# Kernel optimization log

Hardware: AMD Instinct MI355X
Metric: run time of the kernel (lower is better)

The kernel has to match this reference:

```python
import jax, jax.numpy as jnp
import numpy as np

B, T, V, D, P, DEP = 64, 32, 32000, 1024, 8, 4
TAU = 1.0
EPS = 1e-5


def setup_inputs() -> dict:
    key = jax.random.key(0)
    ks = jax.random.split(key, 9)
    s = 0.02
    x = jax.random.randint(ks[0], (B, T), 0, V)
    emb = jax.random.normal(ks[1], (V, D), jnp.float32) * s
    pos = jax.random.normal(ks[2], (T, D), jnp.float32) * s
    # primitive library: n_prims MLPs (Linear -> GELU -> Linear), stacked
    w1 = jax.random.normal(ks[3], (P, D, D), jnp.float32) * s
    b1 = jnp.zeros((P, D), jnp.float32)
    w2 = jax.random.normal(ks[4], (P, D, D), jnp.float32) * s
    b2 = jnp.zeros((P, D), jnp.float32)
    # one selector Linear(dim, n_prims) per depth
    sel_w = jax.random.normal(ks[5], (DEP, P, D), jnp.float32) * s
    sel_b = jnp.zeros((DEP, P), jnp.float32)
    ln_g = jnp.ones((D,), jnp.float32)
    ln_b = jnp.zeros((D,), jnp.float32)
    head_w = jax.random.normal(ks[6], (V, D), jnp.float32) * s
    # fixed gumbel noise (replaces torch's in-op sampling, kept deterministic)
    u = jax.random.uniform(ks[7], (DEP, B, P), jnp.float32, 1e-6, 1.0 - 1e-6)
    gumbel = -jnp.log(-jnp.log(u))
    return dict(x=x, emb=emb, pos=pos, w1=w1, b1=b1, w2=w2, b2=b2,
                sel_w=sel_w, sel_b=sel_b, ln_g=ln_g, ln_b=ln_b,
                head_w=head_w, gumbel=gumbel)


def reference(x, emb, pos, w1, b1, w2, b2, sel_w, sel_b, ln_g, ln_b, head_w, gumbel):
    h = emb[x] + pos[None, :x.shape[1], :]          # [B,T,D]
    div = jnp.float32(0.0)
    unif = jnp.float32(1.0 / P)
    for d in range(DEP):
        ctx = h.mean(axis=1)                         # [B,D]
        logits = ctx @ sel_w[d].T + sel_b[d]         # [B,P]
        weights = jax.nn.softmax((logits + gumbel[d]) / TAU, axis=-1)
        # all primitives over all tokens at once (grouped GEMM), no T loop
        u1 = jax.nn.gelu(jnp.einsum('btd,pde->btpe', h, w1) + b1, approximate=False)
        prim = jnp.einsum('btpe,pef->btpf', u1, w2) + b2   # [B,T,P,D]
        h = h + jnp.einsum('btpf,bp->btf', prim, weights)  # residual add
        avg = weights.mean(axis=0)                   # [P]
        # F.kl_div(avg.log(), uniform, reduction='sum')
        div = div + jnp.sum(unif * (jnp.log(unif) - jnp.log(avg)))
    mu = h.mean(-1, keepdims=True)
    var = ((h - mu) ** 2).mean(-1, keepdims=True)
    hn = (h - mu) * jax.lax.rsqrt(var + EPS) * ln_g + ln_b
    return hn @ head_w.T, div
```

## Files before the change

### kernel.cpp

```cpp
#include <hip/hip_runtime.h>
#include <hip/hip_bf16.h>
#include <math.h>

typedef __bf16 bf16x8 __attribute__((ext_vector_type(8)));
typedef float  f32x4  __attribute__((ext_vector_type(4)));

struct __align__(8) bf16x4s { __hip_bfloat16 a, b, c, d; };

__device__ __forceinline__ void gload_lds16(const void* g, void* l) {
  __builtin_amdgcn_global_load_lds(
      (const __attribute__((address_space(1))) void*)g,
      (__attribute__((address_space(3))) void*)l, 16, 0, 0);
}

__device__ __forceinline__ float fast_gelu(float v) {
  float s = 0.70710678118654752f * v;
  float a = fabsf(s);
  float t = __builtin_amdgcn_rcpf(fmaf(0.3275911f, a, 1.0f));
  float p = t * fmaf(t, fmaf(t, fmaf(t, fmaf(t, 1.061405429f, -1.453152027f),
                                     1.421413741f), -0.284496736f), 0.254829592f);
  float e = __expf(-a * a);
  float er = copysignf(fmaf(-p, e, 1.0f), s);
  return 0.5f * v * (1.0f + er);
}

#define BAR()   asm volatile("s_barrier" ::: "memory")
#define LGKM0() do { asm volatile("s_waitcnt lgkmcnt(0)" ::: "memory"); \
                     __builtin_amdgcn_sched_barrier(0); } while (0)
#define LGKM8() do { asm volatile("s_waitcnt lgkmcnt(8)" ::: "memory"); \
                     __builtin_amdgcn_sched_barrier(0); } while (0)
#define VMC(N)  do { asm volatile("s_waitcnt vmcnt(" #N ")" ::: "memory"); \
                     __builtin_amdgcn_sched_barrier(0); } while (0)
#define P1()    __builtin_amdgcn_s_setprio(1)
#define P0()    __builtin_amdgcn_s_setprio(0)

#define MQ(MB, NB, AV, BV)                                                    \
  do {                                                                        \
    _Pragma("unroll")                                                         \
    for (int mi_ = 0; mi_ < 4; ++mi_)                                         \
      _Pragma("unroll")                                                       \
      for (int nj_ = 0; nj_ < 2; ++nj_)                                       \
        _Pragma("unroll")                                                     \
        for (int kk_ = 0; kk_ < 2; ++kk_)                                     \
          acc[MB + mi_][NB + nj_] = __builtin_amdgcn_mfma_f32_16x16x32_bf16(  \
              AV[mi_][kk_], BV[nj_][kk_], acc[MB + mi_][NB + nj_], 0, 0, 0);  \
  } while (0)

template<int EPI>
__global__ __launch_bounds__(512, 2)
void gemm_nt(const __hip_bfloat16* __restrict__ A,
             const __hip_bfloat16* __restrict__ B,
             const int K, const int Kc, const int N,
             const float* __restrict__ p0,
             const float* __restrict__ p1,
             float* __restrict__ f32out,
             __hip_bfloat16* __restrict__ bfout)
{
  __shared__ __align__(16) __hip_bfloat16 lds[65536];

  const int tid = threadIdx.x;
  const int lane = tid & 63, wid = tid >> 6;
  const int l15 = lane & 15, l4 = lane >> 4;
  const int r8 = lane >> 3, blk = lane & 7;
  const int wm = wid >> 2, wn = wid & 3;

  const int nx = gridDim.x;
  const int flat = blockIdx.x + nx * blockIdx.y;
  const int q = (nx * gridDim.y) >> 3;
  const int nid = (flat & 7) * q + (flat >> 3);
  const long m0 = (long)(nid % nx) * 256;
  const long n0 = (long)(nid / nx) * 256;

  const int kbeg = blockIdx.z * Kc;
  const int nt = Kc / 64;

  f32x4 acc[8][4] = {};
  bf16x8 arE[4][2], arL[4][2], brE[2][2], brL[2][2];

  auto stageA = [&](int buf, int h, int k0) {
#pragma unroll
    for (int p2 = 0; p2 < 2; ++p2) {
      int ch = p2 * 16 + h * 8 + wid;
      int row = ch * 8 + r8;
      gload_lds16(A + (m0 + row) * (long)K + k0 + ((blk ^ r8) << 3),
                  lds + buf * 16384 + ch * 512);
    }
  };
  auto stageB = [&](int buf, int h, int k0) {
#pragma unroll
    for (int p2 = 0; p2 < 2; ++p2) {
      int ch = (p2 * 2 + (wid >> 2)) * 8 + h * 4 + (wid & 3);
      int row = ch * 8 + r8;
      gload_lds16(B + (n0 + row) * (long)K + k0 + ((blk ^ r8) << 3),
                  lds + 32768 + buf * 16384 + ch * 512);
    }
  };
  auto readAE = [&](int buf) {
    const __hip_bfloat16* pA = lds + buf * 16384;
#pragma unroll
    for (int mi = 0; mi < 4; ++mi)
#pragma unroll
      for (int kk = 0; kk < 2; ++kk) {
        int row = wm * 128 + mi * 16 + l15;
        arE[mi][kk] = *(const bf16x8*)(pA + row * 64 + (((kk * 4 + l4) ^ (row & 7)) << 3));
      }
  };
  auto readAL = [&](int buf) {
    const __hip_bfloat16* pA = lds + buf * 16384;
#pragma unroll
    for (int mi = 0; mi < 4; ++mi)
#pragma unroll
      for (int kk = 0; kk < 2; ++kk) {
        int row = wm * 128 + 64 + mi * 16 + l15;
        arL[mi][kk] = *(const bf16x8*)(pA + row * 64 + (((kk * 4 + l4) ^ (row & 7)) << 3));
      }
  };
  auto readBE = [&](int buf) {
    const __hip_bfloat16* pB = lds + 32768 + buf * 16384;
#pragma unroll
    for (int nj = 0; nj < 2; ++nj)
#pragma unroll
      for (int kk = 0; kk < 2; ++kk) {
        int row = wn * 64 + nj * 16 + l15;
        brE[nj][kk] = *(const bf16x8*)(pB + row * 64 + (((kk * 4 + l4) ^ (row & 7)) << 3));
      }
  };
  auto readBL = [&](int buf) {
    const __hip_bfloat16* pB = lds + 32768 + buf * 16384;
#pragma unroll
    for (int nj = 0; nj < 2; ++nj)
#pragma unroll
      for (int kk = 0; kk < 2; ++kk) {
        int row = wn * 64 + 32 + nj * 16 + l15;
        brL[nj][kk] = *(const bf16x8*)(pB + row * 64 + (((kk * 4 + l4) ^ (row & 7)) << 3));
      }
  };

  stageA(0, 0, kbeg); stageB(0, 0, kbeg); stageB(0, 1, kbeg); stageA(0, 1, kbeg);
  VMC(4);
  stageA(1, 0, kbeg + 64); stageB(1, 0, kbeg + 64); stageB(1, 1, kbeg + 64);
  VMC(6);
  BAR();

  const int nit = nt >> 1;
  for (int t = 0; t < nit; ++t) {
    const bool fl = (t + 1 < nit);
    const int kA = kbeg + (2 * t + 1) * 64;
    const int kB = kbeg + (2 * t + 2) * 64;
    const int kC = kbeg + (2 * t + 3) * 64;
    readAE(0); readBE(0);
    stageA(1, 1, kA);
    LGKM8();
    BAR(); LGKM0();
    P1(); MQ(0, 0, arE, brE); P0();
    BAR();
    readBL(0);
    if (fl) stageA(0, 0, kB);
    BAR(); LGKM0();
    P1(); MQ(0, 2, arE, brL); P0();
    BAR();
    readAL(0);
    if (fl) stageB(0, 0, kB);
    BAR(); LGKM0();
    P1(); MQ(4, 0, arL, brE); P0();
    BAR();
    if (fl) stageB(0, 1, kB);
    BAR();
    P1(); MQ(4, 2, arL, brL); P0();
    if (fl) { VMC(6); } else { VMC(0); }
    BAR();
    readAE(1); readBE(1);
    if (fl) stageA(0, 1, kB);
    LGKM8();
    BAR(); LGKM0();
    P1(); MQ(0, 0, arE, brE); P0();
    BAR();
    readBL(1);
    if (fl) stageA(1, 0, kC);
    BAR(); LGKM0();
    P1(); MQ(0, 2, arE, brL); P0();
    BAR();
    readAL(1);
    if (fl) stageB(1, 0, kC);
    BAR(); LGKM0();
    P1(); MQ(4, 0, arL, brE); P0();
    BAR();
    if (fl) stageB(1, 1, kC);
    BAR();
    P1(); MQ(4, 2, arL, brL); P0();
    if (fl) VMC(6);
    BAR();
  }

  const long slab = (EPI == 4) ? (long)blockIdx.z * (long)(gridDim.x * 256) * N : 0;
#pragma unroll
  for (int mi = 0; mi < 8; ++mi) {
    const long gmb = m0 + wm * 128 + mi * 16 + l4 * 4;
    const int b = (int)(gmb >> 5);
#pragma unroll
    for (int nj = 0; nj < 4; ++nj) {
      const long gn = n0 + wn * 64 + nj * 16 + l15;
      if constexpr (EPI == 0) {
        const int p = (int)(gn >> 10), e = (int)(gn & 1023);
        const float bias = p0[(p << 10) + e];
        const float wpb = p1[(b << 3) + p];
#pragma unroll
        for (int r = 0; r < 4; ++r) {
          float v = fast_gelu(acc[mi][nj][r] + bias) * wpb;
          bfout[(gmb + r) * (long)N + gn] = __float2bfloat16(v);
        }
      } else if constexpr (EPI == 2) {
#pragma unroll
        for (int r = 0; r < 4; ++r)
          f32out[(gmb + r) * (long)N + gn] = acc[mi][nj][r];
      } else {
#pragma unroll
        for (int r = 0; r < 4; ++r)
          bfout[slab + (gmb + r) * (long)N + gn] = __float2bfloat16(acc[mi][nj][r]);
      }
    }
  }
}

__global__ void cvt_bf16_k(const float* __restrict__ in, __hip_bfloat16* __restrict__ out, long n) {
  long i = ((long)blockIdx.x * blockDim.x + threadIdx.x) * 4;
  if (i >= n) return;
  float4 v = *(const float4*)(in + i);
  *(bf16x4s*)(out + i) = bf16x4s{__float2bfloat16(v.x), __float2bfloat16(v.y),
                                 __float2bfloat16(v.z), __float2bfloat16(v.w)};
}

__global__ void tconv_k(const float* __restrict__ in, __hip_bfloat16* __restrict__ out,
                        long in_bs, long out_rs, long out_bs) {
  __shared__ float tile[32][33];
  int p = blockIdx.z;
  int r0 = blockIdx.y * 32, c0 = blockIdx.x * 32;
  int tx = threadIdx.x, ty = threadIdx.y;
#pragma unroll
  for (int i = 0; i < 32; i += 8)
    tile[ty + i][tx] = in[(long)p * in_bs + (long)(r0 + ty + i) * 1024 + c0 + tx];
  __syncthreads();
#pragma unroll
  for (int i = 0; i < 32; i += 8)
    out[(long)(c0 + ty + i) * out_rs + (long)p * out_bs + (r0 + tx)] =
        __float2bfloat16(tile[tx][ty + i]);
}

__global__ void embed_k(const int* __restrict__ x, const float* __restrict__ emb,
                        const float* __restrict__ pos, float* __restrict__ h,
                        __hip_bfloat16* __restrict__ hb, float* __restrict__ divp) {
  int row = blockIdx.x;
  int t = row & 31;
  int c = threadIdx.x * 4;
  long tok = x[row];
  float4 e = *(const float4*)(emb + tok * 1024 + c);
  float4 q = *(const float4*)(pos + (long)t * 1024 + c);
  float4 v{e.x + q.x, e.y + q.y, e.z + q.z, e.w + q.w};
  *(float4*)(h + (long)row * 1024 + c) = v;
  *(bf16x4s*)(hb + (long)row * 1024 + c) =
      bf16x4s{__float2bfloat16(v.x), __float2bfloat16(v.y),
              __float2bfloat16(v.z), __float2bfloat16(v.w)};
  if (row == 0 && threadIdx.x == 0) *divp = 0.f;
}

__global__ void select_wb2_k(const float* __restrict__ h, const float* __restrict__ selw,
                             const float* __restrict__ selb, const float* __restrict__ gum,
                             const float* __restrict__ b2, float* __restrict__ W,
                             float* __restrict__ wb2, int dep) {
  int b = blockIdx.x, tid = threadIdx.x;
  int c = tid * 4;
  float4 s{0.f, 0.f, 0.f, 0.f};
  for (int t = 0; t < 32; ++t) {
    const float4 v = *(const float4*)(h + ((long)(b * 32 + t)) * 1024 + c);
    s.x += v.x; s.y += v.y; s.z += v.z; s.w += v.w;
  }
  float lp[8];
#pragma unroll
  for (int p = 0; p < 8; ++p) {
    const float4 w = *(const float4*)(selw + dep * 8192 + p * 1024 + c);
    lp[p] = (s.x * w.x + s.y * w.y + s.z * w.z + s.w * w.w) * (1.f / 32.f);
  }
  int lane = tid & 63, wid = tid >> 6;
#pragma unroll
  for (int p = 0; p < 8; ++p)
    for (int o = 32; o; o >>= 1) lp[p] += __shfl_down(lp[p], o);
  __shared__ float red[4][8];
  __shared__ float wsm[8];
  if (lane == 0) {
#pragma unroll
    for (int p = 0; p < 8; ++p) red[wid][p] = lp[p];
  }
  __syncthreads();
  if (tid == 0) {
    float lg[8], mx = -1e30f;
    for (int p = 0; p < 8; ++p) {
      lg[p] = red[0][p] + red[1][p] + red[2][p] + red[3][p]
            + selb[dep * 8 + p] + gum[dep * 512 + b * 8 + p];
      mx = fmaxf(mx, lg[p]);
    }
    float sm = 0.f;
    for (int p = 0; p < 8; ++p) { lg[p] = expf(lg[p] - mx); sm += lg[p]; }
    float inv = 1.f / sm;
    for (int p = 0; p < 8; ++p) { wsm[p] = lg[p] * inv; W[dep * 512 + b * 8 + p] = lg[p] * inv; }
  }
  __syncthreads();
  float4 a{0.f, 0.f, 0.f, 0.f};
#pragma unroll
  for (int p = 0; p < 8; ++p) {
    float wp = wsm[p];
    const float4 v = *(const float4*)(b2 + p * 1024 + c);
    a.x += wp * v.x; a.y += wp * v.y; a.z += wp * v.z; a.w += wp * v.w;
  }
  *(float4*)(wb2 + (long)b * 1024 + c) = a;
}

__global__ void h_update_k(const __hip_bfloat16* __restrict__ part, float* __restrict__ h,
                           const float* __restrict__ wb2, __hip_bfloat16* __restrict__ hb,
                           const float* __restrict__ Wd, float* __restrict__ divp) {
  int row = blockIdx.x * 2 + (threadIdx.x >> 7);
  int c = (threadIdx.x & 127) * 8;
  long idx = (long)row * 1024 + c;
  float4 a0 = *(const float4*)(h + idx);
  float4 a1 = *(const float4*)(h + idx + 4);
  const float4 w0 = *(const float4*)(wb2 + (long)(row >> 5) * 1024 + c);
  const float4 w1 = *(const float4*)(wb2 + (long)(row >> 5) * 1024 + c + 4);
  a0.x += w0.x; a0.y += w0.y; a0.z += w0.z; a0.w += w0.w;
  a1.x += w1.x; a1.y += w1.y; a1.z += w1.z; a1.w += w1.w;
#pragma unroll
  for (int s = 0; s < 8; ++s) {
    const bf16x8 v = *(const bf16x8*)(part + (long)s * 2097152 + idx);
    a0.x += (float)v[0]; a0.y += (float)v[1]; a0.z += (float)v[2]; a0.w += (float)v[3];
    a1.x += (float)v[4]; a1.y += (float)v[5]; a1.z += (float)v[6]; a1.w += (float)v[7];
  }
  *(float4*)(h + idx) = a0;
  *(float4*)(h + idx + 4) = a1;
  bf16x8 ob;
  ob[0] = (__bf16)a0.x; ob[1] = (__bf16)a0.y; ob[2] = (__bf16)a0.z; ob[3] = (__bf16)a0.w;
  ob[4] = (__bf16)a1.x; ob[5] = (__bf16)a1.y; ob[6] = (__bf16)a1.z; ob[7] = (__bf16)a1.w;
  *(bf16x8*)(hb + idx) = ob;
  if (blockIdx.x == 0 && threadIdx.x < 64) {
    float w8[8];
#pragma unroll
    for (int p = 0; p < 8; ++p) w8[p] = Wd[threadIdx.x * 8 + p];
#pragma unroll
    for (int p = 0; p < 8; ++p)
      for (int o = 32; o; o >>= 1) w8[p] += __shfl_down(w8[p], o);
    if (threadIdx.x == 0) {
      float d = *divp;
      const float u = 0.125f, lu = logf(0.125f);
#pragma unroll
      for (int p = 0; p < 8; ++p) d += u * (lu - logf(w8[p] * (1.f / 64.f)));
      *divp = d;
    }
  }
}

__global__ void ln_k(const float* __restrict__ h, const float* __restrict__ g,
                     const float* __restrict__ be, __hip_bfloat16* __restrict__ hnb,
                     const float* __restrict__ divp, float* __restrict__ divout) {
  int row = blockIdx.x, tid = threadIdx.x;
  int c = tid * 4;
  const float4 v = *(const float4*)(h + (long)row * 1024 + c);
  float s = v.x + v.y + v.z + v.w;
  float q = v.x * v.x + v.y * v.y + v.z * v.z + v.w * v.w;
  for (int o = 32; o; o >>= 1) { s += __shfl_down(s, o); q += __shfl_down(q, o); }
  __shared__ float red[16];
  int lane = tid & 63, wid = tid >> 6;
  if (lane == 0) { red[wid] = s; red[8 + wid] = q; }
  __syncthreads();
  if (tid == 0) {
    float S = red[0] + red[1] + red[2] + red[3];
    float Q = red[8] + red[9] + red[10] + red[11];
    float mu = S * (1.f / 1024.f);
    float var = Q * (1.f / 1024.f) - mu * mu;
    red[0] = mu; red[1] = rsqrtf(var + 1e-5f);
  }
  __syncthreads();
  float mu = red[0], rs = red[1];
  float4 gg = *(const float4*)(g + c), bb = *(const float4*)(be + c);
  *(bf16x4s*)(hnb + (long)row * 1024 + c) =
      bf16x4s{__float2bfloat16((v.x - mu) * rs * gg.x + bb.x),
              __float2bfloat16((v.y - mu) * rs * gg.y + bb.y),
              __float2bfloat16((v.z - mu) * rs * gg.z + bb.z),
              __float2bfloat16((v.w - mu) * rs * gg.w + bb.w)};
  if (row == 0 && tid == 0) *divout = *divp;
}

extern "C" void kernel_launch(void* const* d_in, const int* in_sizes, int n_in,
                              void* d_out, int out_size, void* d_ws, size_t ws_size,
                              hipStream_t stream) {
  (void)in_sizes; (void)n_in; (void)out_size; (void)ws_size;
  const int*   x     = (const int*)  d_in[0];
  const float* emb   = (const float*)d_in[1];
  const float* pos   = (const float*)d_in[2];
  const float* w1    = (const float*)d_in[3];
  const float* b1    = (const float*)d_in[4];
  const float* w2    = (const float*)d_in[5];
  const float* b2    = (const float*)d_in[6];
  const float* selw  = (const float*)d_in[7];
  const float* selb  = (const float*)d_in[8];
  const float* lng   = (const float*)d_in[9];
  const float* lnb   = (const float*)d_in[10];
  const float* headw = (const float*)d_in[11];
  const float* gum   = (const float*)d_in[12];
  float* out = (float*)d_out;

  char* ws = (char*)d_ws;
  __hip_bfloat16* w1t   = (__hip_bfloat16*)(ws);
  __hip_bfloat16* w2t   = (__hip_bfloat16*)(ws + 16777216);
  __hip_bfloat16* headb = (__hip_bfloat16*)(ws + 33554432);
  float*          h     = (float*)(ws + 99090432);
  __hip_bfloat16* hb    = (__hip_bfloat16*)(ws + 107479040);
  __hip_bfloat16* u1    = (__hip_bfloat16*)(ws + 111673344);
  float*          Wall  = (float*)(ws + 145227776);
  float*          wb2   = (float*)(ws + 145240064);
  float*          divp  = (float*)(ws + 145502208);
  __hip_bfloat16* part  = (__hip_bfloat16*)out;

  cvt_bf16_k<<<32000, 256, 0, stream>>>(headw, headb, 32768000L);
  tconv_k<<<dim3(32, 32, 8), dim3(32, 8), 0, stream>>>(w1, w1t, 1L << 20, 1024L, 1L << 20);
  tconv_k<<<dim3(32, 32, 8), dim3(32, 8), 0, stream>>>(w2, w2t, 1L << 20, 8192L, 1024L);
  embed_k<<<2048, 256, 0, stream>>>(x, emb, pos, h, hb, divp);

  for (int d = 0; d < 4; ++d) {
    select_wb2_k<<<64, 256, 0, stream>>>(h, selw, selb, gum, b2, Wall, wb2, d);
    gemm_nt<0><<<dim3(8, 32), 512, 0, stream>>>(hb, w1t, 1024, 1024, 8192, b1, Wall + d * 512, nullptr, u1);
    gemm_nt<4><<<dim3(8, 4, 8), 512, 0, stream>>>(u1, w2t, 8192, 1024, 1024, nullptr, nullptr, nullptr, part);
    h_update_k<<<1024, 256, 0, stream>>>(part, h, wb2, hb, Wall + d * 512, divp);
  }

  ln_k<<<2048, 256, 0, stream>>>(h, lng, lnb, hb, divp, out + 65536000L);
  gemm_nt<2><<<dim3(8, 125), 512, 0, stream>>>(hb, headb, 1024, 1024, 32000, nullptr, nullptr, out, nullptr);
}
```

Baseline: 606.9 us.

## Add dedicated head GEMM loading B operand directly to registers

Replaces the generic gemm_nt instantiation for the final vocabulary projection with a specialized gemm_head kernel. Only the A (activation) tile is staged through LDS, double-buffered with swizzling. The B (head weight) fragments are loaded straight from global memory into registers, also double-buffered, and a flat-to-tile swizzle groups blocks for L2 reuse. This halves the LDS footprint and removes LDS round-trips for B, at the cost of higher register pressure (launch bounds drop to 1 block per CU) and uncoalesced global B reads.

```diff
diff --git a/kernel.cpp b/kernel.cpp
--- a/kernel.cpp
+++ b/kernel.cpp
@@ -46,6 +46,18 @@
               AV[mi_][kk_], BV[nj_][kk_], acc[MB + mi_][NB + nj_], 0, 0, 0);  \
   } while (0)
 
+#define MQH(MB, NB, AV, BV)                                                   \
+  do {                                                                        \
+    _Pragma("unroll")                                                         \
+    for (int mi_ = 0; mi_ < 4; ++mi_)                                         \
+      _Pragma("unroll")                                                       \
+      for (int nj_ = 0; nj_ < 2; ++nj_)                                       \
+        _Pragma("unroll")                                                     \
+        for (int kk_ = 0; kk_ < 2; ++kk_)                                     \
+          acc[MB + mi_][NB + nj_] = __builtin_amdgcn_mfma_f32_16x16x32_bf16(  \
+              AV[mi_][kk_], BV[NB + nj_][kk_], acc[MB + mi_][NB + nj_], 0, 0, 0); \
+  } while (0)
+
 template<int EPI>
 __global__ __launch_bounds__(512, 2)
 void gemm_nt(const __hip_bfloat16* __restrict__ A,
@@ -209,15 +221,130 @@
           float v = fast_gelu(acc[mi][nj][r] + bias) * wpb;
           bfout[(gmb + r) * (long)N + gn] = __float2bfloat16(v);
         }
-      } else if constexpr (EPI == 2) {
-#pragma unroll
-        for (int r = 0; r < 4; ++r)
-          f32out[(gmb + r) * (long)N + gn] = acc[mi][nj][r];
       } else {
 #pragma unroll
         for (int r = 0; r < 4; ++r)
           bfout[slab + (gmb + r) * (long)N + gn] = __float2bfloat16(acc[mi][nj][r]);
       }
+    }
+  }
+}
+
+__global__ __launch_bounds__(512, 1)
+void gemm_head(const __hip_bfloat16* __restrict__ A,
+               const __hip_bfloat16* __restrict__ B,
+               const int K, const int N, float* __restrict__ f32out)
+{
+  __shared__ __align__(16) __hip_bfloat16 lds[32768];
+
+  const int tid = threadIdx.x;
+  const int lane = tid & 63, wid = tid >> 6;
+  const int l15 = lane & 15, l4 = lane >> 4;
+  const int r8 = lane >> 3, blk = lane & 7;
+  const int wm = wid >> 2, wn = wid & 3;
+
+  const int nx = gridDim.x;
+  const int flat = blockIdx.x + nx * blockIdx.y;
+  const int q = (nx * gridDim.y) >> 3;
+  const int nid = (flat & 7) * q + (flat >> 3);
+  const long m0 = (long)(nid % nx) * 256;
+  const long n0 = (long)(nid / nx) * 256;
+
+  const int nt = K / 64;
+
+  f32x4 acc[8][4] = {};
+  bf16x8 ar[4][2];
+  bf16x8 b0[4][2], b1[4][2];
+
+  auto stageA2 = [&](int buf, int k0) {
+#pragma unroll
+    for (int p2 = 0; p2 < 4; ++p2) {
+      int ch = p2 * 8 + wid;
+      int row = ch * 8 + r8;
+      gload_lds16(A + (m0 + row) * (long)K + k0 + ((blk ^ r8) << 3),
+                  lds + buf * 16384 + ch * 512);
+    }
+  };
+  auto loadB = [&](bf16x8 (&bb)[4][2], int k0) {
+#pragma unroll
+    for (int nj = 0; nj < 4; ++nj)
+#pragma unroll
+      for (int kk = 0; kk < 2; ++kk)
+        bb[nj][kk] = *(const bf16x8*)(B + (n0 + wn * 64 + nj * 16 + l15) * (long)K
+                                        + k0 + kk * 32 + l4 * 8);
+  };
+  auto readAE = [&](int buf) {
+    const __hip_bfloat16* pA = lds + buf * 16384;
+#pragma unroll
+    for (int mi = 0; mi < 4; ++mi)
+#pragma unroll
+      for (int kk = 0; kk < 2; ++kk) {
+        int row = wm * 128 + mi * 16 + l15;
+        ar[mi][kk] = *(const bf16x8*)(pA + row * 64 + (((kk * 4 + l4) ^ (row & 7)) << 3));
+      }
+  };
+  auto readAL = [&](int buf) {
+    const __hip_bfloat16* pA = lds + buf * 16384;
+#pragma unroll
+    for (int mi = 0; mi < 4; ++mi)
+#pragma unroll
+      for (int kk = 0; kk < 2; ++kk) {
+        int row = wm * 128 + 64 + mi * 16 + l15;
+        ar[mi][kk] = *(const bf16x8*)(pA + row * 64 + (((kk * 4 + l4) ^ (row & 7)) << 3));
+      }
+  };
+
+  stageA2(0, 0);
+  loadB(b0, 0);
+  stageA2(1, 64);
+  VMC(12);
+  BAR();
+  readAE(0);
+
+  const int nit = nt >> 1;
+  for (int t = 0; t < nit - 1; ++t) {
+    loadB(b1, (2 * t + 1) * 64);
+    P1(); MQH(0, 0, ar, b0); MQH(0, 2, ar, b0); P0();
+    readAL(0);
+    P1(); MQH(4, 0, ar, b0); MQH(4, 2, ar, b0); P0();
+    LGKM0();
+    BAR();
+    stageA2(0, (2 * t + 2) * 64);
+    VMC(12);
+    BAR();
+    readAE(1);
+    loadB(b0, (2 * t + 2) * 64);
+    P1(); MQH(0, 0, ar, b1); MQH(0, 2, ar, b1); P0();
+    readAL(1);
+    P1(); MQH(4, 0, ar, b1); MQH(4, 2, ar, b1); P0();
+    LGKM0();
+    BAR();
+    stageA2(1, (2 * t + 3) * 64);
+    VMC(12);
+    BAR();
+    readAE(0);
+  }
+
+  loadB(b1, (nt - 1) * 64);
+  P1(); MQH(0, 0, ar, b0); MQH(0, 2, ar, b0); P0();
+  readAL(0);
+  P1(); MQH(4, 0, ar, b0); MQH(4, 2, ar, b0); P0();
+  VMC(8);
+  BAR();
+  readAE(1);
+  P1(); MQH(0, 0, ar, b1); MQH(0, 2, ar, b1); P0();
+  readAL(1);
+  P1(); MQH(4, 0, ar, b1); MQH(4, 2, ar, b1); P0();
+
+#pragma unroll
+  for (int mi = 0; mi < 8; ++mi) {
+    const long gmb = m0 + wm * 128 + mi * 16 + l4 * 4;
+#pragma unroll
+    for (int nj = 0; nj < 4; ++nj) {
+      const long gn = n0 + wn * 64 + nj * 16 + l15;
+#pragma unroll
+      for (int r = 0; r < 4; ++r)
+        f32out[(gmb + r) * (long)N + gn] = acc[mi][nj][r];
     }
   }
 }
@@ -430,5 +557,5 @@
   }
 
   ln_k<<<2048, 256, 0, stream>>>(h, lng, lnb, hb, divp, out + 65536000L);
-  gemm_nt<2><<<dim3(8, 125), 512, 0, stream>>>(hb, headb, 1024, 1024, 32000, nullptr, nullptr, out, nullptr);
-}
+  gemm_head<<<dim3(8, 125), 512, 0, stream>>>(hb, headb, 1024, 32000, out);
+}
```

New measurement: 707.7 us. +16.6%, slower.
